# Kernel optimization log

Hardware: AMD Instinct MI355X
Metric: run time of the kernel (lower is better)

The kernel has to match this reference:

```python
import jax, jax.numpy as jnp
import numpy as np

N = 50000   # nodes
E = 800000  # edges
H = 128     # hidden dim
V = 50000   # feats_per_node (embedding vocab)


def setup_inputs() -> dict:
    key = jax.random.key(0)
    ks = jax.random.split(key, 16)
    s = 0.05  # keep activations in a sane range
    return {
        "node_ids": jax.random.randint(ks[0], (N,), 0, V),
        "src": jax.random.randint(ks[1], (E,), 0, N),
        "dst": jnp.sort(jax.random.randint(ks[2], (E,), 0, N)),
        "emb": jax.random.normal(ks[3], (V, H), jnp.float32) * s,
        "W_pool1": jax.random.normal(ks[4], (H, H), jnp.float32) * s,
        "b_pool1": jax.random.normal(ks[5], (H,), jnp.float32) * s,
        "W_self1": jax.random.normal(ks[6], (H, H), jnp.float32) * s,
        "W_neigh1": jax.random.normal(ks[7], (H, H), jnp.float32) * s,
        "b1": jax.random.normal(ks[8], (H,), jnp.float32) * s,
        "W_pool2": jax.random.normal(ks[9], (H, H), jnp.float32) * s,
        "b_pool2": jax.random.normal(ks[10], (H,), jnp.float32) * s,
        "W_self2": jax.random.normal(ks[11], (H, H), jnp.float32) * s,
        "W_neigh2": jax.random.normal(ks[12], (H, H), jnp.float32) * s,
        "b2": jax.random.normal(ks[13], (H,), jnp.float32) * s,
    }


def _sage_pool_layer(h, src, dst, W_pool, b_pool, W_self, W_neigh, b):
    # DGL SAGEConv('pool'): per-src MLP, gather over edges, segmented max per dst.
    m = jax.nn.relu(h @ W_pool + b_pool)              # [N, H]
    msgs = m[src]                                     # [E, H] gather
    agg = jax.ops.segment_max(msgs, dst, num_segments=N,
                              indices_are_sorted=True)  # [N, H]
    agg = jnp.where(jnp.isneginf(agg), 0.0, agg)      # zero-in-degree -> 0 (DGL semantics)
    return h @ W_self + agg @ W_neigh + b


def reference(node_ids, src, dst, emb,
              W_pool1, b_pool1, W_self1, W_neigh1, b1,
              W_pool2, b_pool2, W_self2, W_neigh2, b2):
    h = emb[node_ids]                                 # embedding_h on 1-hot indices
    h = _sage_pool_layer(h, src, dst, W_pool1, b_pool1, W_self1, W_neigh1, b1)
    h = _sage_pool_layer(h, src, dst, W_pool2, b_pool2, W_self2, W_neigh2, b2)
    return h
```

## Files before the change

kernel.cpp:

```cpp
#include <hip/hip_runtime.h>

#define HD 128

typedef __attribute__((ext_vector_type(8))) short short8;
typedef __attribute__((ext_vector_type(4))) float floatx4;

typedef unsigned short ushort_t;
typedef unsigned int uint_t;

__device__ __forceinline__ ushort_t f2b(float f) {
    union { float f; uint_t u; } v; v.f = f;
    uint_t r = v.u + 0x7fff + ((v.u >> 16) & 1);
    return (ushort_t)(r >> 16);
}
__device__ __forceinline__ float b_lo(uint_t p) {
    union { uint_t u; float f; } v; v.u = p << 16; return v.f;
}
__device__ __forceinline__ float b_hi(uint_t p) {
    union { uint_t u; float f; } v; v.u = p & 0xffff0000u; return v.f;
}
__device__ __forceinline__ uint_t packb(float a, float b) {
    union { float f; uint_t u; } x, y; x.f = a; y.f = b;
    return (x.u >> 16) | (y.u & 0xffff0000u);
}
__device__ __forceinline__ short8 cvt8(const float* __restrict__ p) {
    float4 u = *(const float4*)p, v = *(const float4*)(p + 4);
    short8 r;
    r[0] = (short)f2b(u.x); r[1] = (short)f2b(u.y); r[2] = (short)f2b(u.z); r[3] = (short)f2b(u.w);
    r[4] = (short)f2b(v.x); r[5] = (short)f2b(v.y); r[6] = (short)f2b(v.z); r[7] = (short)f2b(v.w);
    return r;
}

__global__ __launch_bounds__(256) void k_prep(const int* __restrict__ dst, int E,
                                              int* __restrict__ rp, int N,
                                              const float* W0, const float* W1,
                                              const float* W2, const float* W3,
                                              const float* W4, const float* W5,
                                              ushort_t* __restrict__ Wpk, int nbR) {
    int b = blockIdx.x;
    if (b < nbR) {
        int i = b * 256 + threadIdx.x;
        if (i > N) return;
        int lo = 0, hi = E;
        while (lo < hi) {
            int mid = (lo + hi) >> 1;
            if (dst[mid] < i) lo = mid + 1; else hi = mid;
        }
        rp[i] = lo;
    } else {
        int bb = b - nbR;
        const float* Ws[6] = {W0, W1, W2, W3, W4, W5};
        int mat = bb >> 6;
        int o = ((bb & 63) << 8) + threadIdx.x;
        int j = o & 7, l = (o >> 3) & 63, s = (o >> 9) & 3, t = o >> 11;
        int k = s * 32 + ((l >> 4) & 3) * 8 + j;
        int n = t * 16 + (l & 15);
        Wpk[(size_t)mat * 16384 + o] = f2b(Ws[mat][k * HD + n]);
    }
}

__device__ __forceinline__ void stage_w(const ushort_t* __restrict__ g,
                                        ushort_t* l, int tid) {
#pragma unroll
    for (int i = 0; i < 8; ++i) {
        int off = i * 2048 + tid * 8;
        *(short8*)&l[off] = *(const short8*)&g[off];
    }
}

__device__ __forceinline__ void store_bf16(ushort_t* __restrict__ m, int row,
                                           int colbase, const floatx4& acc,
                                           const float4& bv, bool relu, int N) {
    if (row >= N) return;
    float v0 = acc[0] + bv.x, v1 = acc[1] + bv.y, v2 = acc[2] + bv.z, v3 = acc[3] + bv.w;
    if (relu) { v0 = fmaxf(v0, 0.f); v1 = fmaxf(v1, 0.f); v2 = fmaxf(v2, 0.f); v3 = fmaxf(v3, 0.f); }
    uint2 o; o.x = (uint_t)f2b(v0) | ((uint_t)f2b(v1) << 16);
    o.y = (uint_t)f2b(v2) | ((uint_t)f2b(v3) << 16);
    *(uint2*)&m[(size_t)row * HD + colbase] = o;
}

__global__ __launch_bounds__(256) void k_gather_pool(const int* __restrict__ ids,
                                                     const float* __restrict__ emb,
                                                     const ushort_t* __restrict__ Wpk,
                                                     const float* __restrict__ bias,
                                                     ushort_t* __restrict__ h0,
                                                     ushort_t* __restrict__ m, int N) {
    __shared__ ushort_t Wl[16384];
    int wave = blockIdx.x * 4 + (threadIdx.x >> 6);
    int row0 = wave * 32;
    int l = threadIdx.x & 63;
    int ar0 = row0 + (l & 15); if (ar0 >= N) ar0 = N - 1;
    int ar1 = ar0 + 16;        if (ar1 >= N) ar1 = N - 1;
    int ac = (l >> 4) * 8;
    int id0 = ids[ar0], id1 = ids[ar1];
    short8 a0[4], a1[4];
#pragma unroll
    for (int s = 0; s < 4; ++s) {
        a0[s] = cvt8(&emb[(size_t)id0 * HD + s * 32 + ac]);
        a1[s] = cvt8(&emb[(size_t)id1 * HD + s * 32 + ac]);
    }
    stage_w(Wpk, Wl, threadIdx.x);
    __syncthreads();
    if (row0 >= N) return;
#pragma unroll
    for (int s = 0; s < 4; ++s) {
        *(short8*)&h0[(size_t)ar0 * HD + s * 32 + ac] = a0[s];
        *(short8*)&h0[(size_t)ar1 * HD + s * 32 + ac] = a1[s];
    }
    int g0 = row0 + (l & 15), g1 = g0 + 16;
    int cb0 = ((l >> 4) & 3) * 4;
#pragma unroll
    for (int t = 0; t < 8; ++t) {
        floatx4 acc0 = {0.f, 0.f, 0.f, 0.f};
        floatx4 acc1 = {0.f, 0.f, 0.f, 0.f};
#pragma unroll
        for (int s = 0; s < 4; ++s) {
            short8 w = *(const short8*)&Wl[(t * 4 + s) * 512 + l * 8];
            acc0 = __builtin_amdgcn_mfma_f32_16x16x32_bf16(w, a0[s], acc0, 0, 0, 0);
            acc1 = __builtin_amdgcn_mfma_f32_16x16x32_bf16(w, a1[s], acc1, 0, 0, 0);
        }
        int cb = t * 16 + cb0;
        float4 bv = *(const float4*)&bias[cb];
        store_bf16(m, g0, cb, acc0, bv, true, N);
        store_bf16(m, g1, cb, acc1, bv, true, N);
    }
}

__global__ __launch_bounds__(256) void k_pool(const ushort_t* __restrict__ h,
                                              const ushort_t* __restrict__ Wpk,
                                              const float* __restrict__ bias,
                                              ushort_t* __restrict__ m, int N) {
    __shared__ ushort_t Wl[16384];
    int wave = blockIdx.x * 4 + (threadIdx.x >> 6);
    int row0 = wave * 32;
    int l = threadIdx.x & 63;
    int ar0 = row0 + (l & 15); if (ar0 >= N) ar0 = N - 1;
    int ar1 = ar0 + 16;        if (ar1 >= N) ar1 = N - 1;
    int ac = (l >> 4) * 8;
    short8 a0[4], a1[4];
#pragma unroll
    for (int s = 0; s < 4; ++s) {
        a0[s] = *(const short8*)&h[(size_t)ar0 * HD + s * 32 + ac];
        a1[s] = *(const short8*)&h[(size_t)ar1 * HD + s * 32 + ac];
    }
    stage_w(Wpk, Wl, threadIdx.x);
    __syncthreads();
    if (row0 >= N) return;
    int g0 = row0 + (l & 15), g1 = g0 + 16;
    int cb0 = ((l >> 4) & 3) * 4;
#pragma unroll
    for (int t = 0; t < 8; ++t) {
        floatx4 acc0 = {0.f, 0.f, 0.f, 0.f};
        floatx4 acc1 = {0.f, 0.f, 0.f, 0.f};
#pragma unroll
        for (int s = 0; s < 4; ++s) {
            short8 w = *(const short8*)&Wl[(t * 4 + s) * 512 + l * 8];
            acc0 = __builtin_amdgcn_mfma_f32_16x16x32_bf16(w, a0[s], acc0, 0, 0, 0);
            acc1 = __builtin_amdgcn_mfma_f32_16x16x32_bf16(w, a1[s], acc1, 0, 0, 0);
        }
        int cb = t * 16 + cb0;
        float4 bv = *(const float4*)&bias[cb];
        store_bf16(m, g0, cb, acc0, bv, true, N);
        store_bf16(m, g1, cb, acc1, bv, true, N);
    }
}

__global__ __launch_bounds__(256) void k_segmax(const ushort_t* __restrict__ m,
                                                const int* __restrict__ src,
                                                const int* __restrict__ rp,
                                                ushort_t* __restrict__ agg, int N) {
    int node = blockIdx.x * 4 + (threadIdx.x >> 6);
    if (node >= N) return;
    int l = threadIdx.x & 63;
    int slot = l >> 4;
    int col8 = (l & 15) * 8;
    int beg = rp[node], end = rp[node + 1];
    float a[8] = {0.f, 0.f, 0.f, 0.f, 0.f, 0.f, 0.f, 0.f};
    float c[8] = {0.f, 0.f, 0.f, 0.f, 0.f, 0.f, 0.f, 0.f};
    for (int base = beg; base < end; base += 64) {
        int nb = end - base; if (nb > 64) nb = 64;
        int si = base + l; if (si > end - 1) si = end - 1;
        int sv = src[si];
        for (int o = 0; o < nb; o += 16) {
            int last = nb - 1;
            int i0 = o + slot;      if (i0 > last) i0 = last;
            int i1 = o + 4 + slot;  if (i1 > last) i1 = last;
            int i2 = o + 8 + slot;  if (i2 > last) i2 = last;
            int i3 = o + 12 + slot; if (i3 > last) i3 = last;
            int s0 = __shfl(sv, i0), s1 = __shfl(sv, i1);
            int s2 = __shfl(sv, i2), s3 = __shfl(sv, i3);
            uint4 p0 = *(const uint4*)&m[(size_t)s0 * HD + col8];
            uint4 p1 = *(const uint4*)&m[(size_t)s1 * HD + col8];
            uint4 p2 = *(const uint4*)&m[(size_t)s2 * HD + col8];
            uint4 p3 = *(const uint4*)&m[(size_t)s3 * HD + col8];
            a[0] = fmaxf(a[0], b_lo(p0.x)); a[1] = fmaxf(a[1], b_hi(p0.x));
            a[2] = fmaxf(a[2], b_lo(p0.y)); a[3] = fmaxf(a[3], b_hi(p0.y));
            a[4] = fmaxf(a[4], b_lo(p0.z)); a[5] = fmaxf(a[5], b_hi(p0.z));
            a[6] = fmaxf(a[6], b_lo(p0.w)); a[7] = fmaxf(a[7], b_hi(p0.w));
            c[0] = fmaxf(c[0], b_lo(p1.x)); c[1] = fmaxf(c[1], b_hi(p1.x));
            c[2] = fmaxf(c[2], b_lo(p1.y)); c[3] = fmaxf(c[3], b_hi(p1.y));
            c[4] = fmaxf(c[4], b_lo(p1.z)); c[5] = fmaxf(c[5], b_hi(p1.z));
            c[6] = fmaxf(c[6], b_lo(p1.w)); c[7] = fmaxf(c[7], b_hi(p1.w));
            a[0] = fmaxf(a[0], b_lo(p2.x)); a[1] = fmaxf(a[1], b_hi(p2.x));
            a[2] = fmaxf(a[2], b_lo(p2.y)); a[3] = fmaxf(a[3], b_hi(p2.y));
            a[4] = fmaxf(a[4], b_lo(p2.z)); a[5] = fmaxf(a[5], b_hi(p2.z));
            a[6] = fmaxf(a[6], b_lo(p2.w)); a[7] = fmaxf(a[7], b_hi(p2.w));
            c[0] = fmaxf(c[0], b_lo(p3.x)); c[1] = fmaxf(c[1], b_hi(p3.x));
            c[2] = fmaxf(c[2], b_lo(p3.y)); c[3] = fmaxf(c[3], b_hi(p3.y));
            c[4] = fmaxf(c[4], b_lo(p3.z)); c[5] = fmaxf(c[5], b_hi(p3.z));
            c[6] = fmaxf(c[6], b_lo(p3.w)); c[7] = fmaxf(c[7], b_hi(p3.w));
        }
    }
#pragma unroll
    for (int i = 0; i < 8; ++i) {
        a[i] = fmaxf(a[i], c[i]);
        a[i] = fmaxf(a[i], __shfl_xor(a[i], 16));
        a[i] = fmaxf(a[i], __shfl_xor(a[i], 32));
    }
    if (slot == 0) {
        uint4 o;
        o.x = packb(a[0], a[1]); o.y = packb(a[2], a[3]);
        o.z = packb(a[4], a[5]); o.w = packb(a[6], a[7]);
        *(uint4*)&agg[(size_t)node * HD + col8] = o;
    }
}

template <bool F32OUT>
__global__ __launch_bounds__(256) void k_dual(const ushort_t* __restrict__ h,
                                              const ushort_t* __restrict__ agg,
                                              const ushort_t* __restrict__ WsPk,
                                              const ushort_t* __restrict__ WnPk,
                                              const float* __restrict__ bias,
                                              void* __restrict__ outp, int N) {
    __shared__ ushort_t Wl[32768];
    int wave = blockIdx.x * 4 + (threadIdx.x >> 6);
    int row0 = wave * 32;
    int l = threadIdx.x & 63;
    int ar0 = row0 + (l & 15); if (ar0 >= N) ar0 = N - 1;
    int ar1 = ar0 + 16;        if (ar1 >= N) ar1 = N - 1;
    int ac = (l >> 4) * 8;
    short8 ah0[4], ah1[4], ag0[4], ag1[4];
#pragma unroll
    for (int s = 0; s < 4; ++s) {
        ah0[s] = *(const short8*)&h[(size_t)ar0 * HD + s * 32 + ac];
        ah1[s] = *(const short8*)&h[(size_t)ar1 * HD + s * 32 + ac];
        ag0[s] = *(const short8*)&agg[(size_t)ar0 * HD + s * 32 + ac];
        ag1[s] = *(const short8*)&agg[(size_t)ar1 * HD + s * 32 + ac];
    }
    stage_w(WsPk, Wl, threadIdx.x);
    stage_w(WnPk, Wl + 16384, threadIdx.x);
    __syncthreads();
    if (row0 >= N) return;
    int g0 = row0 + (l & 15), g1 = g0 + 16;
    int cb0 = ((l >> 4) & 3) * 4;
#pragma unroll
    for (int t = 0; t < 8; ++t) {
        floatx4 acc0 = {0.f, 0.f, 0.f, 0.f};
        floatx4 acc1 = {0.f, 0.f, 0.f, 0.f};
#pragma unroll
        for (int s = 0; s < 4; ++s) {
            short8 ws = *(const short8*)&Wl[(t * 4 + s) * 512 + l * 8];
            acc0 = __builtin_amdgcn_mfma_f32_16x16x32_bf16(ws, ah0[s], acc0, 0, 0, 0);
            acc1 = __builtin_amdgcn_mfma_f32_16x16x32_bf16(ws, ah1[s], acc1, 0, 0, 0);
        }
#pragma unroll
        for (int s = 0; s < 4; ++s) {
            short8 wn = *(const short8*)&Wl[16384 + (t * 4 + s) * 512 + l * 8];
            acc0 = __builtin_amdgcn_mfma_f32_16x16x32_bf16(wn, ag0[s], acc0, 0, 0, 0);
            acc1 = __builtin_amdgcn_mfma_f32_16x16x32_bf16(wn, ag1[s], acc1, 0, 0, 0);
        }
        int cb = t * 16 + cb0;
        float4 bv = *(const float4*)&bias[cb];
        if (F32OUT) {
            float* out = (float*)outp;
            if (g0 < N) {
                float4 v = make_float4(acc0[0] + bv.x, acc0[1] + bv.y,
                                       acc0[2] + bv.z, acc0[3] + bv.w);
                *(float4*)&out[(size_t)g0 * HD + cb] = v;
            }
            if (g1 < N) {
                float4 v = make_float4(acc1[0] + bv.x, acc1[1] + bv.y,
                                       acc1[2] + bv.z, acc1[3] + bv.w);
                *(float4*)&out[(size_t)g1 * HD + cb] = v;
            }
        } else {
            ushort_t* out = (ushort_t*)outp;
            store_bf16(out, g0, cb, acc0, bv, false, N);
            store_bf16(out, g1, cb, acc1, bv, false, N);
        }
    }
}

extern "C" void kernel_launch(void* const* d_in, const int* in_sizes, int n_in,
                              void* d_out, int out_size, void* d_ws, size_t ws_size,
                              hipStream_t stream) {
    const int*   node_ids = (const int*)d_in[0];
    const int*   src      = (const int*)d_in[1];
    const int*   dst      = (const int*)d_in[2];
    const float* emb      = (const float*)d_in[3];
    const float* Wp1      = (const float*)d_in[4];
    const float* bp1      = (const float*)d_in[5];
    const float* Ws1      = (const float*)d_in[6];
    const float* Wn1      = (const float*)d_in[7];
    const float* b1       = (const float*)d_in[8];
    const float* Wp2      = (const float*)d_in[9];
    const float* bp2      = (const float*)d_in[10];
    const float* Ws2      = (const float*)d_in[11];
    const float* Wn2      = (const float*)d_in[12];
    const float* b2       = (const float*)d_in[13];
    float* out = (float*)d_out;

    const int N = in_sizes[0];
    const int E = in_sizes[1];

    char* ws = (char*)d_ws;
    int* rp = (int*)ws;
    size_t off = (((size_t)(N + 1) * 4) + 255) & ~(size_t)255;
    ushort_t* Wpk  = (ushort_t*)(ws + off);
    ushort_t* h0   = Wpk + 6 * 16384;
    ushort_t* h1   = h0 + (size_t)N * HD;
    ushort_t* bufM = h1 + (size_t)N * HD;
    ushort_t* bufA = bufM + (size_t)N * HD;

    const int nbR = (N + 1 + 255) / 256;
    const int nbP = 6 * 64;
    const int nb_gemm = (N + 127) / 128;
    const int nb_seg  = (N + 3) / 4;

    k_prep<<<nbR + nbP, 256, 0, stream>>>(dst, E, rp, N,
                                          Wp1, Ws1, Wn1, Wp2, Ws2, Wn2, Wpk, nbR);

    const ushort_t* Wp1k = Wpk;
    const ushort_t* Ws1k = Wpk + 16384;
    const ushort_t* Wn1k = Wpk + 2 * 16384;
    const ushort_t* Wp2k = Wpk + 3 * 16384;
    const ushort_t* Ws2k = Wpk + 4 * 16384;
    const ushort_t* Wn2k = Wpk + 5 * 16384;

    k_gather_pool<<<nb_gemm, 256, 0, stream>>>(node_ids, emb, Wp1k, bp1, h0, bufM, N);
    k_segmax<<<nb_seg, 256, 0, stream>>>(bufM, src, rp, bufA, N);
    k_dual<false><<<nb_gemm, 256, 0, stream>>>(h0, bufA, Ws1k, Wn1k, b1, h1, N);
    k_pool<<<nb_gemm, 256, 0, stream>>>(h1, Wp2k, bp2, bufM, N);
    k_segmax<<<nb_seg, 256, 0, stream>>>(bufM, src, rp, bufA, N);
    k_dual<true><<<nb_gemm, 256, 0, stream>>>(h1, bufA, Ws2k, Wn2k, b2, out, N);
}
```

Before: 214.3 us.

## Split segment-max feature columns across four blocks per node group

The segmented max kernel now launches four times as many blocks, each handling a 32-column slice of the feature row for four nodes. Each lane loads 8 bytes instead of 16 and processes 8 edges in parallel instead of 4, with one extra shuffle-reduction step. The aim is more parallelism and latency hiding for the gather-bound reduction. The cost is reading the src indices four times, more, smaller memory requests, and more blocks to launch.

```diff
diff --git a/kernel.cpp b/kernel.cpp
--- a/kernel.cpp
+++ b/kernel.cpp
@@ -169,59 +169,42 @@
                                                 const int* __restrict__ src,
                                                 const int* __restrict__ rp,
                                                 ushort_t* __restrict__ agg, int N) {
-    int node = blockIdx.x * 4 + (threadIdx.x >> 6);
+    int slice = blockIdx.x & 3;
+    int node = (blockIdx.x >> 2) * 4 + (threadIdx.x >> 6);
     if (node >= N) return;
     int l = threadIdx.x & 63;
-    int slot = l >> 4;
-    int col8 = (l & 15) * 8;
+    int slot = l >> 3;
+    int colbase = slice * 32 + (l & 7) * 4;
     int beg = rp[node], end = rp[node + 1];
-    float a[8] = {0.f, 0.f, 0.f, 0.f, 0.f, 0.f, 0.f, 0.f};
-    float c[8] = {0.f, 0.f, 0.f, 0.f, 0.f, 0.f, 0.f, 0.f};
+    float a0 = 0.f, a1 = 0.f, a2 = 0.f, a3 = 0.f;
+    float c0 = 0.f, c1 = 0.f, c2 = 0.f, c3 = 0.f;
     for (int base = beg; base < end; base += 64) {
         int nb = end - base; if (nb > 64) nb = 64;
         int si = base + l; if (si > end - 1) si = end - 1;
         int sv = src[si];
         for (int o = 0; o < nb; o += 16) {
             int last = nb - 1;
-            int i0 = o + slot;      if (i0 > last) i0 = last;
-            int i1 = o + 4 + slot;  if (i1 > last) i1 = last;
-            int i2 = o + 8 + slot;  if (i2 > last) i2 = last;
-            int i3 = o + 12 + slot; if (i3 > last) i3 = last;
+            int i0 = o + slot;     if (i0 > last) i0 = last;
+            int i1 = o + 8 + slot; if (i1 > last) i1 = last;
             int s0 = __shfl(sv, i0), s1 = __shfl(sv, i1);
-            int s2 = __shfl(sv, i2), s3 = __shfl(sv, i3);
-            uint4 p0 = *(const uint4*)&m[(size_t)s0 * HD + col8];
-            uint4 p1 = *(const uint4*)&m[(size_t)s1 * HD + col8];
-            uint4 p2 = *(const uint4*)&m[(size_t)s2 * HD + col8];
-            uint4 p3 = *(const uint4*)&m[(size_t)s3 * HD + col8];
-            a[0] = fmaxf(a[0], b_lo(p0.x)); a[1] = fmaxf(a[1], b_hi(p0.x));
-            a[2] = fmaxf(a[2], b_lo(p0.y)); a[3] = fmaxf(a[3], b_hi(p0.y));
-            a[4] = fmaxf(a[4], b_lo(p0.z)); a[5] = fmaxf(a[5], b_hi(p0.z));
-            a[6] = fmaxf(a[6], b_lo(p0.w)); a[7] = fmaxf(a[7], b_hi(p0.w));
-            c[0] = fmaxf(c[0], b_lo(p1.x)); c[1] = fmaxf(c[1], b_hi(p1.x));
-            c[2] = fmaxf(c[2], b_lo(p1.y)); c[3] = fmaxf(c[3], b_hi(p1.y));
-            c[4] = fmaxf(c[4], b_lo(p1.z)); c[5] = fmaxf(c[5], b_hi(p1.z));
-            c[6] = fmaxf(c[6], b_lo(p1.w)); c[7] = fmaxf(c[7], b_hi(p1.w));
-            a[0] = fmaxf(a[0], b_lo(p2.x)); a[1] = fmaxf(a[1], b_hi(p2.x));
-            a[2] = fmaxf(a[2], b_lo(p2.y)); a[3] = fmaxf(a[3], b_hi(p2.y));
-            a[4] = fmaxf(a[4], b_lo(p2.z)); a[5] = fmaxf(a[5], b_hi(p2.z));
-            a[6] = fmaxf(a[6], b_lo(p2.w)); a[7] = fmaxf(a[7], b_hi(p2.w));
-            c[0] = fmaxf(c[0], b_lo(p3.x)); c[1] = fmaxf(c[1], b_hi(p3.x));
-            c[2] = fmaxf(c[2], b_lo(p3.y)); c[3] = fmaxf(c[3], b_hi(p3.y));
-            c[4] = fmaxf(c[4], b_lo(p3.z)); c[5] = fmaxf(c[5], b_hi(p3.z));
-            c[6] = fmaxf(c[6], b_lo(p3.w)); c[7] = fmaxf(c[7], b_hi(p3.w));
-        }
-    }
-#pragma unroll
-    for (int i = 0; i < 8; ++i) {
-        a[i] = fmaxf(a[i], c[i]);
-        a[i] = fmaxf(a[i], __shfl_xor(a[i], 16));
-        a[i] = fmaxf(a[i], __shfl_xor(a[i], 32));
-    }
+            uint2 p0 = *(const uint2*)&m[(size_t)s0 * HD + colbase];
+            uint2 p1 = *(const uint2*)&m[(size_t)s1 * HD + colbase];
+            a0 = fmaxf(a0, b_lo(p0.x)); a1 = fmaxf(a1, b_hi(p0.x));
+            a2 = fmaxf(a2, b_lo(p0.y)); a3 = fmaxf(a3, b_hi(p0.y));
+            c0 = fmaxf(c0, b_lo(p1.x)); c1 = fmaxf(c1, b_hi(p1.x));
+            c2 = fmaxf(c2, b_lo(p1.y)); c3 = fmaxf(c3, b_hi(p1.y));
+        }
+    }
+    a0 = fmaxf(a0, c0); a1 = fmaxf(a1, c1); a2 = fmaxf(a2, c2); a3 = fmaxf(a3, c3);
+    a0 = fmaxf(a0, __shfl_xor(a0, 8));  a1 = fmaxf(a1, __shfl_xor(a1, 8));
+    a2 = fmaxf(a2, __shfl_xor(a2, 8));  a3 = fmaxf(a3, __shfl_xor(a3, 8));
+    a0 = fmaxf(a0, __shfl_xor(a0, 16)); a1 = fmaxf(a1, __shfl_xor(a1, 16));
+    a2 = fmaxf(a2, __shfl_xor(a2, 16)); a3 = fmaxf(a3, __shfl_xor(a3, 16));
+    a0 = fmaxf(a0, __shfl_xor(a0, 32)); a1 = fmaxf(a1, __shfl_xor(a1, 32));
+    a2 = fmaxf(a2, __shfl_xor(a2, 32)); a3 = fmaxf(a3, __shfl_xor(a3, 32));
     if (slot == 0) {
-        uint4 o;
-        o.x = packb(a[0], a[1]); o.y = packb(a[2], a[3]);
-        o.z = packb(a[4], a[5]); o.w = packb(a[6], a[7]);
-        *(uint4*)&agg[(size_t)node * HD + col8] = o;
+        uint2 o; o.x = packb(a0, a1); o.y = packb(a2, a3);
+        *(uint2*)&agg[(size_t)node * HD + colbase] = o;
     }
 }
 
@@ -325,7 +308,7 @@
     const int nbR = (N + 1 + 255) / 256;
     const int nbP = 6 * 64;
     const int nb_gemm = (N + 127) / 128;
-    const int nb_seg  = (N + 3) / 4;
+    const int nb_seg  = ((N + 3) / 4) * 4;
 
     k_prep<<<nbR + nbP, 256, 0, stream>>>(dst, E, rp, N,
                                           Wp1, Ws1, Wn1, Wp2, Ws2, Wn2, Wpk, nbR);
```

Measured after the change: 294.4 us. 37.4% more time.

## Use packed u16 max for bf16 segmax and prewarm message buffer in cache

Applied to the files above, without the earlier changes.

The segmented max now works directly on packed bf16 words with v_pk_max_u16 instead of unpacking to float, fmaxf-ing and repacking. This is valid because all messages are non-negative after ReLU, so unsigned integer ordering matches float ordering. A new streaming kernel reads the whole message buffer before each segmax, to pull it into the large last-level cache so the later random gathers hit in cache. The cost is an extra launch and a full read of the buffer, and the integer max relies on the ReLU invariant.

```diff
diff --git a/kernel.cpp b/kernel.cpp
--- a/kernel.cpp
+++ b/kernel.cpp
@@ -12,16 +12,6 @@
     union { float f; uint_t u; } v; v.f = f;
     uint_t r = v.u + 0x7fff + ((v.u >> 16) & 1);
     return (ushort_t)(r >> 16);
-}
-__device__ __forceinline__ float b_lo(uint_t p) {
-    union { uint_t u; float f; } v; v.u = p << 16; return v.f;
-}
-__device__ __forceinline__ float b_hi(uint_t p) {
-    union { uint_t u; float f; } v; v.u = p & 0xffff0000u; return v.f;
-}
-__device__ __forceinline__ uint_t packb(float a, float b) {
-    union { float f; uint_t u; } x, y; x.f = a; y.f = b;
-    return (x.u >> 16) | (y.u & 0xffff0000u);
 }
 __device__ __forceinline__ short8 cvt8(const float* __restrict__ p) {
     float4 u = *(const float4*)p, v = *(const float4*)(p + 4);
@@ -29,6 +19,17 @@
     r[0] = (short)f2b(u.x); r[1] = (short)f2b(u.y); r[2] = (short)f2b(u.z); r[3] = (short)f2b(u.w);
     r[4] = (short)f2b(v.x); r[5] = (short)f2b(v.y); r[6] = (short)f2b(v.z); r[7] = (short)f2b(v.w);
     return r;
+}
+__device__ __forceinline__ uint_t pkmax(uint_t a, uint_t b) {
+    uint_t d;
+    asm("v_pk_max_u16 %0, %1, %2" : "=v"(d) : "v"(a), "v"(b));
+    return d;
+}
+__device__ __forceinline__ uint4 pkmax4(uint4 a, uint4 b) {
+    uint4 d;
+    d.x = pkmax(a.x, b.x); d.y = pkmax(a.y, b.y);
+    d.z = pkmax(a.z, b.z); d.w = pkmax(a.w, b.w);
+    return d;
 }
 
 __global__ __launch_bounds__(256) void k_prep(const int* __restrict__ dst, int E,
@@ -77,6 +78,17 @@
     uint2 o; o.x = (uint_t)f2b(v0) | ((uint_t)f2b(v1) << 16);
     o.y = (uint_t)f2b(v2) | ((uint_t)f2b(v3) << 16);
     *(uint2*)&m[(size_t)row * HD + colbase] = o;
+}
+
+__global__ __launch_bounds__(256) void k_warm(const uint4* __restrict__ p, int n4,
+                                              uint_t* __restrict__ sink) {
+    uint_t acc = 0;
+    int stride = gridDim.x * 256;
+    for (int i = blockIdx.x * 256 + threadIdx.x; i < n4; i += stride) {
+        uint4 v = p[i];
+        acc ^= v.x ^ v.y ^ v.z ^ v.w;
+    }
+    if (acc == 0xDEADBEEFu) sink[blockIdx.x] = acc;
 }
 
 __global__ __launch_bounds__(256) void k_gather_pool(const int* __restrict__ ids,
@@ -175,8 +187,7 @@
     int slot = l >> 4;
     int col8 = (l & 15) * 8;
     int beg = rp[node], end = rp[node + 1];
-    float a[8] = {0.f, 0.f, 0.f, 0.f, 0.f, 0.f, 0.f, 0.f};
-    float c[8] = {0.f, 0.f, 0.f, 0.f, 0.f, 0.f, 0.f, 0.f};
+    uint4 A = {0u, 0u, 0u, 0u}, C = {0u, 0u, 0u, 0u};
     for (int base = beg; base < end; base += 64) {
         int nb = end - base; if (nb > 64) nb = 64;
         int si = base + l; if (si > end - 1) si = end - 1;
@@ -193,36 +204,20 @@
             uint4 p1 = *(const uint4*)&m[(size_t)s1 * HD + col8];
             uint4 p2 = *(const uint4*)&m[(size_t)s2 * HD + col8];
             uint4 p3 = *(const uint4*)&m[(size_t)s3 * HD + col8];
-            a[0] = fmaxf(a[0], b_lo(p0.x)); a[1] = fmaxf(a[1], b_hi(p0.x));
-            a[2] = fmaxf(a[2], b_lo(p0.y)); a[3] = fmaxf(a[3], b_hi(p0.y));
-            a[4] = fmaxf(a[4], b_lo(p0.z)); a[5] = fmaxf(a[5], b_hi(p0.z));
-            a[6] = fmaxf(a[6], b_lo(p0.w)); a[7] = fmaxf(a[7], b_hi(p0.w));
-            c[0] = fmaxf(c[0], b_lo(p1.x)); c[1] = fmaxf(c[1], b_hi(p1.x));
-            c[2] = fmaxf(c[2], b_lo(p1.y)); c[3] = fmaxf(c[3], b_hi(p1.y));
-            c[4] = fmaxf(c[4], b_lo(p1.z)); c[5] = fmaxf(c[5], b_hi(p1.z));
-            c[6] = fmaxf(c[6], b_lo(p1.w)); c[7] = fmaxf(c[7], b_hi(p1.w));
-            a[0] = fmaxf(a[0], b_lo(p2.x)); a[1] = fmaxf(a[1], b_hi(p2.x));
-            a[2] = fmaxf(a[2], b_lo(p2.y)); a[3] = fmaxf(a[3], b_hi(p2.y));
-            a[4] = fmaxf(a[4], b_lo(p2.z)); a[5] = fmaxf(a[5], b_hi(p2.z));
-            a[6] = fmaxf(a[6], b_lo(p2.w)); a[7] = fmaxf(a[7], b_hi(p2.w));
-            c[0] = fmaxf(c[0], b_lo(p3.x)); c[1] = fmaxf(c[1], b_hi(p3.x));
-            c[2] = fmaxf(c[2], b_lo(p3.y)); c[3] = fmaxf(c[3], b_hi(p3.y));
-            c[4] = fmaxf(c[4], b_lo(p3.z)); c[5] = fmaxf(c[5], b_hi(p3.z));
-            c[6] = fmaxf(c[6], b_lo(p3.w)); c[7] = fmaxf(c[7], b_hi(p3.w));
-        }
-    }
-#pragma unroll
-    for (int i = 0; i < 8; ++i) {
-        a[i] = fmaxf(a[i], c[i]);
-        a[i] = fmaxf(a[i], __shfl_xor(a[i], 16));
-        a[i] = fmaxf(a[i], __shfl_xor(a[i], 32));
-    }
-    if (slot == 0) {
-        uint4 o;
-        o.x = packb(a[0], a[1]); o.y = packb(a[2], a[3]);
-        o.z = packb(a[4], a[5]); o.w = packb(a[6], a[7]);
-        *(uint4*)&agg[(size_t)node * HD + col8] = o;
-    }
+            A = pkmax4(A, p0); C = pkmax4(C, p1);
+            A = pkmax4(A, p2); C = pkmax4(C, p3);
+        }
+    }
+    A = pkmax4(A, C);
+#pragma unroll
+    for (int d = 16; d <= 32; d <<= 1) {
+        uint4 t;
+        t.x = (uint_t)__shfl_xor((int)A.x, d); t.y = (uint_t)__shfl_xor((int)A.y, d);
+        t.z = (uint_t)__shfl_xor((int)A.z, d); t.w = (uint_t)__shfl_xor((int)A.w, d);
+        A = pkmax4(A, t);
+    }
+    if (slot == 0)
+        *(uint4*)&agg[(size_t)node * HD + col8] = A;
 }
 
 template <bool F32OUT>
@@ -321,11 +316,13 @@
     ushort_t* h1   = h0 + (size_t)N * HD;
     ushort_t* bufM = h1 + (size_t)N * HD;
     ushort_t* bufA = bufM + (size_t)N * HD;
+    uint_t*   sink = (uint_t*)(bufA + (size_t)N * HD);
 
     const int nbR = (N + 1 + 255) / 256;
     const int nbP = 6 * 64;
-    const int nb_gemm = (N + 127) / 128;
-    const int nb_seg  = (N + 3) / 4;
+    const int nbG = (N + 127) / 128;
+    const int nb_seg = (N + 3) / 4;
+    const int n4 = N * HD / 8;
 
     k_prep<<<nbR + nbP, 256, 0, stream>>>(dst, E, rp, N,
                                           Wp1, Ws1, Wn1, Wp2, Ws2, Wn2, Wpk, nbR);
@@ -337,10 +334,12 @@
     const ushort_t* Ws2k = Wpk + 4 * 16384;
     const ushort_t* Wn2k = Wpk + 5 * 16384;
 
-    k_gather_pool<<<nb_gemm, 256, 0, stream>>>(node_ids, emb, Wp1k, bp1, h0, bufM, N);
+    k_gather_pool<<<nbG, 256, 0, stream>>>(node_ids, emb, Wp1k, bp1, h0, bufM, N);
+    k_warm<<<512, 256, 0, stream>>>((const uint4*)bufM, n4, sink);
     k_segmax<<<nb_seg, 256, 0, stream>>>(bufM, src, rp, bufA, N);
-    k_dual<false><<<nb_gemm, 256, 0, stream>>>(h0, bufA, Ws1k, Wn1k, b1, h1, N);
-    k_pool<<<nb_gemm, 256, 0, stream>>>(h1, Wp2k, bp2, bufM, N);
+    k_dual<false><<<nbG, 256, 0, stream>>>(h0, bufA, Ws1k, Wn1k, b1, h1, N);
+    k_pool<<<nbG, 256, 0, stream>>>(h1, Wp2k, bp2, bufM, N);
+    k_warm<<<512, 256, 0, stream>>>((const uint4*)bufM, n4, sink);
     k_segmax<<<nb_seg, 256, 0, stream>>>(bufM, src, rp, bufA, N);
-    k_dual<true><<<nb_gemm, 256, 0, stream>>>(h1, bufA, Ws2k, Wn2k, b2, out, N);
-}
+    k_dual<true><<<nbG, 256, 0, stream>>>(h1, bufA, Ws2k, Wn2k, b2, out, N);
+}
```

Measured after the change: 220.6 us. +2.9%, slower.
